# Kernel tuning notes

Measured on AMD Instinct MI355X. Metric: run time of the kernel, lower is better.

## Reference

```python
import jax, jax.numpy as jnp
import numpy as np

N, E = 100000, 3200000          # nodes, edges (avg degree 32)
F_IN, HID, OUT2, NUM_CLASSES = 128, 64, 2, 4


def setup_inputs() -> dict:
    key = jax.random.key(0)
    ks = jax.random.split(key, 8)
    x = jax.random.normal(ks[0], (N, F_IN), dtype=jnp.float32)
    edge_index = jax.random.randint(ks[1], (2, E), 0, N, dtype=jnp.int32)
    # Glorot-ish inits for the linear weights, zero biases (PyG GCNConv default)
    W1 = jax.random.normal(ks[2], (F_IN, HID), dtype=jnp.float32) / np.float32(np.sqrt(F_IN))
    b1 = jnp.zeros((HID,), jnp.float32)
    W2 = jax.random.normal(ks[3], (HID, OUT2), dtype=jnp.float32) / np.float32(np.sqrt(HID))
    b2 = jnp.zeros((OUT2,), jnp.float32)
    Wc = jax.random.normal(ks[4], (OUT2, NUM_CLASSES), dtype=jnp.float32) / np.float32(np.sqrt(OUT2))
    bc = jnp.zeros((NUM_CLASSES,), jnp.float32)
    return {"x": x, "edge_index": edge_index, "W1": W1, "b1": b1,
            "W2": W2, "b2": b2, "Wc": Wc, "bc": bc}


def gcn_conv(x, W, b, src, dst):
    """PyG GCNConv: out = D^-1/2 (A+I) D^-1/2 (x W) + b, sum aggregation."""
    n = x.shape[0]
    # degree of A+I: 1 (self loop) + in-degree at target nodes
    deg = jnp.ones((n,), x.dtype).at[dst].add(jnp.asarray(1.0, x.dtype))
    dinv = jax.lax.rsqrt(deg)                      # deg >= 1 always
    xw = x @ W                                      # [n, out] dense GEMM first
    norm = dinv[src] * dinv[dst]                    # [E]
    agg = jax.ops.segment_sum(xw[src] * norm[:, None], dst, num_segments=n)
    agg = agg + xw * (dinv * dinv)[:, None]         # self-loop contribution
    return agg + b


def reference(x, edge_index, W1, b1, W2, b2, Wc, bc):
    src, dst = edge_index[0], edge_index[1]
    h = jnp.tanh(gcn_conv(x, W1, b1, src, dst))
    h = jnp.tanh(gcn_conv(h, W2, b2, src, dst))
    out = h @ Wc + bc
    return (out, h)
```

## Files before the change

### kernel.cpp

```cpp
#include <hip/hip_runtime.h>
#include <hip/hip_bf16.h>
#include <hip/hip_fp16.h>


#define NB2 256
#define CAP2 9472
#define MAXB 400
#define BIN_CHUNK 4096

__global__ __launch_bounds__(256) void k_bin(const int* __restrict__ src,
                                             const int* __restrict__ dst,
                                             int E, int nbuckets,
                                             int* __restrict__ binCnt,
                                             int* __restrict__ bins) {
    __shared__ int stageP[BIN_CHUNK];
    __shared__ unsigned short stageB[BIN_CHUNK];
    __shared__ int lcnt[MAXB];
    __shared__ int lbase[MAXB + 1];
    __shared__ int gbase[MAXB];
    __shared__ int lpos[MAXB];
    int base = blockIdx.x * BIN_CHUNK;
    if (base >= E) return;
    int cnt_here = min(BIN_CHUNK, E - base);

    for (int b = threadIdx.x; b < nbuckets; b += 256) lcnt[b] = 0;
    __syncthreads();

    int p_[16], b_[16];
    #pragma unroll
    for (int k = 0; k < 4; k++) {
        int e0 = base + (k * 256 + threadIdx.x) * 4;
        int s4[4], d4[4];
        if (e0 + 3 < E) {
            *reinterpret_cast<int4*>(s4) = *reinterpret_cast<const int4*>(src + e0);
            *reinterpret_cast<int4*>(d4) = *reinterpret_cast<const int4*>(dst + e0);
            #pragma unroll
            for (int j = 0; j < 4; j++) {
                int b = d4[j] >> 8;
                b_[4 * k + j] = b;
                p_[4 * k + j] = s4[j] | ((d4[j] & 255) << 17);
                atomicAdd(&lcnt[b], 1);
            }
        } else {
            #pragma unroll
            for (int j = 0; j < 4; j++) {
                int e = e0 + j;
                if (e < E) {
                    int s = src[e], d = dst[e];
                    int b = d >> 8;
                    b_[4 * k + j] = b;
                    p_[4 * k + j] = s | ((d & 255) << 17);
                    atomicAdd(&lcnt[b], 1);
                } else {
                    b_[4 * k + j] = -1;
                }
            }
        }
    }
    __syncthreads();

    if (threadIdx.x < 64) {
        int lane = threadIdx.x;
        int per = (nbuckets + 63) >> 6;
        int start = lane * per;
        int v[8];
        int s = 0;
        for (int i = 0; i < per; ++i) {
            int b = start + i;
            v[i] = (b < nbuckets) ? lcnt[b] : 0;
            s += v[i];
        }
        int run = s;
        #pragma unroll
        for (int off = 1; off < 64; off <<= 1) {
            int t = __shfl_up(run, off);
            if (lane >= off) run += t;
        }
        int acc = run - s;
        for (int i = 0; i < per; ++i) {
            int b = start + i;
            if (b < nbuckets) lbase[b] = acc;
            acc += v[i];
        }
        if (lane == 63) lbase[nbuckets] = run;
    }
    __syncthreads();
    for (int b = threadIdx.x; b < nbuckets; b += 256) {
        gbase[b] = atomicAdd(&binCnt[b], lcnt[b]);
        lpos[b] = lbase[b];
    }
    __syncthreads();
    #pragma unroll
    for (int k = 0; k < 16; k++) {
        if (b_[k] >= 0) {
            int pos = atomicAdd(&lpos[b_[k]], 1);
            stageP[pos] = p_[k];
            stageB[pos] = (unsigned short)b_[k];
        }
    }
    __syncthreads();
    for (int i = threadIdx.x; i < cnt_here; i += 256) {
        int b = stageB[i];
        int gi = gbase[b] + (i - lbase[b]);
        if (gi < CAP2) bins[(size_t)b * CAP2 + gi] = stageP[i];
    }
}

__global__ void k_bscan(const int* __restrict__ binCnt, int* __restrict__ bbase,
                        int nbuckets, int* __restrict__ rowptr, int N) {
    int lane = threadIdx.x;
    int per = (nbuckets + 63) >> 6;
    int start = lane * per;
    int v[8];
    int s = 0;
    for (int i = 0; i < per; ++i) {
        int b = start + i;
        v[i] = (b < nbuckets) ? min(binCnt[b], CAP2) : 0;
        s += v[i];
    }
    int run = s;
    #pragma unroll
    for (int off = 1; off < 64; off <<= 1) {
        int t = __shfl_up(run, off);
        if (lane >= off) run += t;
    }
    int acc = run - s;
    for (int i = 0; i < per; ++i) {
        int b = start + i;
        if (b < nbuckets) bbase[b] = acc;
        acc += v[i];
    }
    if (lane == 63) {
        bbase[nbuckets] = run;
        rowptr[N] = run;
    }
}

__global__ __launch_bounds__(256) void k_csr(const int* __restrict__ bins,
                                             const int* __restrict__ binCnt,
                                             const int* __restrict__ bbase,
                                             int* __restrict__ rowptr,
                                             int* __restrict__ csr_src,
                                             float* __restrict__ dinv, int N) {
    __shared__ int hist[NB2];
    __shared__ int sc[NB2];
    __shared__ int lcur[NB2];
    __shared__ int stage[CAP2];
    int b = blockIdx.x;
    int lo = b * NB2;
    int nn = min(NB2, N - lo);
    if (nn <= 0) return;
    int m = min(binCnt[b], CAP2);
    const int* bp = bins + (size_t)b * CAP2;
    int t = threadIdx.x;

    hist[t] = 0;
    __syncthreads();
    for (int i = t; i < m; i += 256) {
        unsigned int e = (unsigned int)__builtin_nontemporal_load(bp + i);
        atomicAdd(&hist[e >> 17], 1);
    }
    __syncthreads();
    int h = (t < nn) ? hist[t] : 0;
    sc[t] = h;
    __syncthreads();
    #pragma unroll
    for (int off = 1; off < 256; off <<= 1) {
        int val = sc[t];
        int add = (t >= off) ? sc[t - off] : 0;
        __syncthreads();
        sc[t] = val + add;
        __syncthreads();
    }
    int excl = sc[t] - h;
    int gb = bbase[b];
    if (t < nn) {
        rowptr[lo + t] = gb + excl;
        lcur[t] = excl;
        dinv[lo + t] = rsqrtf(1.0f + (float)h);
    }
    __syncthreads();
    for (int i = t; i < m; i += 256) {
        unsigned int e = (unsigned int)__builtin_nontemporal_load(bp + i);
        int p = atomicAdd(&lcur[e >> 17], 1);
        stage[p] = (int)(e & 0x1FFFF);
    }
    __syncthreads();
    for (int i = t; i < m; i += 256) {
        csr_src[gb + i] = stage[i];
    }
}

__global__ __launch_bounds__(256) void k_gemm1(const float* __restrict__ x,
                                               const float* __restrict__ W1,
                                               const float* __restrict__ dinv,
                                               __half* __restrict__ xw, int n) {
    int lrow = threadIdx.x & 63;
    int c0 = __builtin_amdgcn_readfirstlane((threadIdx.x >> 6) * 16);
    int row = blockIdx.x * 64 + lrow;
    if (row > n) return;
    if (row == n) {
        float4 z = make_float4(0.f, 0.f, 0.f, 0.f);
        float4* op = reinterpret_cast<float4*>(xw + (size_t)row * 64 + c0);
        op[0] = z;
        op[1] = z;
        return;
    }
    const float* xr = x + (size_t)row * 128;

    float acc[16];
    #pragma unroll
    for (int c = 0; c < 16; ++c) acc[c] = 0.f;

    for (int k4 = 0; k4 < 32; ++k4) {
        float4 xv = *reinterpret_cast<const float4*>(xr + k4 * 4);
        const float* wp = W1 + (size_t)k4 * 4 * 64 + c0;
        #pragma unroll
        for (int c = 0; c < 16; ++c) {
            acc[c] = fmaf(xv.x, wp[c], acc[c]);
            acc[c] = fmaf(xv.y, wp[64 + c], acc[c]);
            acc[c] = fmaf(xv.z, wp[128 + c], acc[c]);
            acc[c] = fmaf(xv.w, wp[192 + c], acc[c]);
        }
    }

    float di = dinv[row];
    __half2 hb[8];
    #pragma unroll
    for (int c = 0; c < 8; ++c)
        hb[c] = __floats2half2_rn(acc[2 * c] * di, acc[2 * c + 1] * di);
    float4* op = reinterpret_cast<float4*>(xw + (size_t)row * 64 + c0);
    const float4* hp = reinterpret_cast<const float4*>(hb);
    op[0] = hp[0];
    op[1] = hp[1];
}

__global__ void k_agg1(const int* __restrict__ rowptr, const int* __restrict__ csr_src,
                       const float* __restrict__ dinv, const __half* __restrict__ xw1s,
                       const float* __restrict__ b1, const float* __restrict__ W2,
                       float* __restrict__ xw2s, int n) {
    int lane = threadIdx.x & 63;
    int q    = lane >> 4;
    int ln   = lane & 15;
    float4 b1v = *reinterpret_cast<const float4*>(b1 + 4 * ln);
    float4 w2a = *reinterpret_cast<const float4*>(W2 + 8 * ln);
    float4 w2b = *reinterpret_cast<const float4*>(W2 + 8 * ln + 4);
    const float2* xp2 = reinterpret_cast<const float2*>(xw1s);

    int wid  = blockIdx.x * (blockDim.x >> 6) + (threadIdx.x >> 6);
    int wtot = gridDim.x * (blockDim.x >> 6);
    int nquad = (n + 3) >> 2;
    for (int qd = wid; qd < nquad; qd += wtot) {
        int d = 4 * qd + q;
        bool ok = d < n;
        int base = 0, cnt = 0;
        float dd = 0.f;
        if (ok) { base = rowptr[d]; cnt = rowptr[d + 1] - base; dd = dinv[d]; }
        float a0 = 0.f, a1 = 0.f, a2 = 0.f, a3 = 0.f;

        int nch = (cnt + 15) >> 4;
        int ncm = max(nch, __shfl_xor(nch, 16));
        ncm = max(ncm, __shfl_xor(ncm, 32));

        for (int c = 0; c < ncm; ++c) {
            int rel = c * 16 + ln;
            int v = (rel < cnt) ? __builtin_nontemporal_load(csr_src + base + rel) : n;
            float2 r[16];
            #pragma unroll
            for (int k = 0; k < 16; ++k) {
                int sv = __shfl(v, (q << 4) | k);
                r[k] = xp2[(size_t)sv * 16 + ln];
            }
            __builtin_amdgcn_sched_barrier(0);
            #pragma unroll
            for (int k = 0; k < 16; ++k) {
                float2 f01 = __half22float2(__builtin_bit_cast(__half2, r[k].x));
                float2 f23 = __half22float2(__builtin_bit_cast(__half2, r[k].y));
                a0 += f01.x;
                a1 += f01.y;
                a2 += f23.x;
                a3 += f23.y;
            }
        }

        float p0 = 0.f, p1 = 0.f;
        if (ok) {
            float2 r = xp2[(size_t)d * 16 + ln];
            float2 s01 = __half22float2(__builtin_bit_cast(__half2, r.x));
            float2 s23 = __half22float2(__builtin_bit_cast(__half2, r.y));
            float h0 = tanhf((a0 + s01.x) * dd + b1v.x);
            float h1 = tanhf((a1 + s01.y) * dd + b1v.y);
            float h2 = tanhf((a2 + s23.x) * dd + b1v.z);
            float h3 = tanhf((a3 + s23.y) * dd + b1v.w);
            p0 = h0 * w2a.x + h1 * w2a.z + h2 * w2b.x + h3 * w2b.z;
            p1 = h0 * w2a.y + h1 * w2a.w + h2 * w2b.y + h3 * w2b.w;
        }
        #pragma unroll
        for (int m = 8; m >= 1; m >>= 1) {
            p0 += __shfl_xor(p0, m);
            p1 += __shfl_xor(p1, m);
        }
        if (ok && ln == 0)
            *reinterpret_cast<float2*>(xw2s + (size_t)d * 2) = make_float2(p0 * dd, p1 * dd);
    }
}

__global__ void k_agg2(const int* __restrict__ rowptr, const int* __restrict__ csr_src,
                       const float* __restrict__ dinv, const float* __restrict__ xw2s,
                       const float* __restrict__ b2, const float* __restrict__ Wc,
                       const float* __restrict__ bc,
                       float* __restrict__ out, float* __restrict__ hout, int n) {
    int lane = threadIdx.x & 63;
    int slot = lane >> 1;
    int f = lane & 1;
    float b2v = b2[f];
    int wid = blockIdx.x * (blockDim.x >> 6) + (threadIdx.x >> 6);
    int wtot = gridDim.x * (blockDim.x >> 6);
    for (int d = wid; d < n; d += wtot) {
        int base = rowptr[d], end = rowptr[d + 1];
        float dd = dinv[d];
        float acc = (slot == 0) ? xw2s[(size_t)d * 2 + f] : 0.f;
        for (int j = base + slot; j < end; j += 32) {
            int s = __builtin_nontemporal_load(csr_src + j);
            acc += xw2s[(size_t)s * 2 + f];
        }
        #pragma unroll
        for (int m = 32; m >= 2; m >>= 1) acc += __shfl_xor(acc, m);
        float h = tanhf(acc * dd + b2v);
        float other = __shfl_xor(h, 1);
        if (lane == 0) {
            *reinterpret_cast<float2*>(hout + (size_t)d * 2) = make_float2(h, other);
            float4 o;
            o.x = fmaf(h, Wc[0], fmaf(other, Wc[4], bc[0]));
            o.y = fmaf(h, Wc[1], fmaf(other, Wc[5], bc[1]));
            o.z = fmaf(h, Wc[2], fmaf(other, Wc[6], bc[2]));
            o.w = fmaf(h, Wc[3], fmaf(other, Wc[7], bc[3]));
            *reinterpret_cast<float4*>(out + (size_t)d * 4) = o;
        }
    }
}

extern "C" void kernel_launch(void* const* d_in, const int* in_sizes, int n_in,
                              void* d_out, int out_size, void* d_ws, size_t ws_size,
                              hipStream_t stream) {
    const float* x  = (const float*)d_in[0];
    const int* ei   = (const int*)d_in[1];
    const float* W1 = (const float*)d_in[2];
    const float* b1 = (const float*)d_in[3];
    const float* W2 = (const float*)d_in[4];
    const float* b2 = (const float*)d_in[5];
    const float* Wc = (const float*)d_in[6];
    const float* bc = (const float*)d_in[7];

    const int N = in_sizes[0] / 128;
    const int E = in_sizes[1] / 2;
    const int* src = ei;
    const int* dst = ei + E;

    float* out  = (float*)d_out;
    float* hout = out + (size_t)N * 4;

    const int NBK = (N + NB2 - 1) / NB2;

    char* ws = (char*)d_ws;
    int*    csr_src = (int*)ws;
    char*   uni     = (char*)(csr_src + E);
    int*    bins    = (int*)uni;
    __half* xw1s    = (__half*)uni;
    size_t uni_sz   = (size_t)NBK * CAP2 * sizeof(int);
    size_t xw1_sz   = (size_t)(N + 1) * 64 * sizeof(__half);
    char*  after    = uni + (uni_sz > xw1_sz ? uni_sz : xw1_sz);
    int*   binCnt   = (int*)after;
    int*   bbase    = binCnt + NBK;
    float* dinv     = (float*)(bbase + NBK + 1);
    float* xw2s     = dinv + N;
    int*   rowptr   = (int*)(xw2s + (size_t)N * 2);

    (void)hipMemsetAsync(binCnt, 0, (size_t)NBK * sizeof(int), stream);
    k_bin<<<(E + BIN_CHUNK - 1) / BIN_CHUNK, 256, 0, stream>>>(src, dst, E, NBK, binCnt, bins);
    k_bscan<<<1, 64, 0, stream>>>(binCnt, bbase, NBK, rowptr, N);
    k_csr<<<NBK, 256, 0, stream>>>(bins, binCnt, bbase, rowptr, csr_src, dinv, N);

    k_gemm1<<<(N + 64) / 64, 256, 0, stream>>>(x, W1, dinv, xw1s, N);
    k_agg1<<<2048, 256, 0, stream>>>(rowptr, csr_src, dinv, xw1s, b1, W2, xw2s, N);
    k_agg2<<<2048, 256, 0, stream>>>(rowptr, csr_src, dinv, xw2s, b2, Wc, bc, out, hout, N);
}
```

Before: 188.7 us.

## Sort nodes by degree within buckets for balanced aggregation; widen binning blocks

k_csr now builds a per-bucket counting sort of destination nodes by in-degree (dperm), and k_agg1 processes nodes in that order. Each wavefront's four node groups then have similar edge counts, which cuts idle lanes in the chunk loop where all quarters run to the maximum chunk count. Separately, k_bin moves to 512-thread blocks over 8192-edge chunks, giving fewer blocks and fewer global atomic merges per bucket. The costs are an extra scan in k_csr, an extra indirection load in k_agg1, scattered rather than sequential node access in k_agg1, and more shared memory in k_bin.

```diff
diff --git a/kernel.cpp b/kernel.cpp
--- a/kernel.cpp
+++ b/kernel.cpp
@@ -6,9 +6,9 @@
 #define NB2 256
 #define CAP2 9472
 #define MAXB 400
-#define BIN_CHUNK 4096
-
-__global__ __launch_bounds__(256) void k_bin(const int* __restrict__ src,
+#define BIN_CHUNK 8192
+
+__global__ __launch_bounds__(512) void k_bin(const int* __restrict__ src,
                                              const int* __restrict__ dst,
                                              int E, int nbuckets,
                                              int* __restrict__ binCnt,
@@ -23,13 +23,13 @@
     if (base >= E) return;
     int cnt_here = min(BIN_CHUNK, E - base);
 
-    for (int b = threadIdx.x; b < nbuckets; b += 256) lcnt[b] = 0;
+    for (int b = threadIdx.x; b < nbuckets; b += 512) lcnt[b] = 0;
     __syncthreads();
 
     int p_[16], b_[16];
     #pragma unroll
     for (int k = 0; k < 4; k++) {
-        int e0 = base + (k * 256 + threadIdx.x) * 4;
+        int e0 = base + (k * 512 + threadIdx.x) * 4;
         int s4[4], d4[4];
         if (e0 + 3 < E) {
             *reinterpret_cast<int4*>(s4) = *reinterpret_cast<const int4*>(src + e0);
@@ -85,7 +85,7 @@
         if (lane == 63) lbase[nbuckets] = run;
     }
     __syncthreads();
-    for (int b = threadIdx.x; b < nbuckets; b += 256) {
+    for (int b = threadIdx.x; b < nbuckets; b += 512) {
         gbase[b] = atomicAdd(&binCnt[b], lcnt[b]);
         lpos[b] = lbase[b];
     }
@@ -99,7 +99,7 @@
         }
     }
     __syncthreads();
-    for (int i = threadIdx.x; i < cnt_here; i += 256) {
+    for (int i = threadIdx.x; i < cnt_here; i += 512) {
         int b = stageB[i];
         int gi = gbase[b] + (i - lbase[b]);
         if (gi < CAP2) bins[(size_t)b * CAP2 + gi] = stageP[i];
@@ -141,10 +141,13 @@
                                              const int* __restrict__ bbase,
                                              int* __restrict__ rowptr,
                                              int* __restrict__ csr_src,
-                                             float* __restrict__ dinv, int N) {
+                                             float* __restrict__ dinv,
+                                             int* __restrict__ dperm, int N) {
     __shared__ int hist[NB2];
     __shared__ int sc[NB2];
     __shared__ int lcur[NB2];
+    __shared__ int dh[NB2];
+    __shared__ int dcur[NB2];
     __shared__ int stage[CAP2];
     int b = blockIdx.x;
     int lo = b * NB2;
@@ -155,6 +158,8 @@
     int t = threadIdx.x;
 
     hist[t] = 0;
+    dh[t] = 0;
+    dcur[t] = 0;
     __syncthreads();
     for (int i = t; i < m; i += 256) {
         unsigned int e = (unsigned int)__builtin_nontemporal_load(bp + i);
@@ -162,6 +167,8 @@
     }
     __syncthreads();
     int h = (t < nn) ? hist[t] : 0;
+    int g = min(h, 255);
+    if (t < nn) atomicAdd(&dh[g], 1);
     sc[t] = h;
     __syncthreads();
     #pragma unroll
@@ -180,6 +187,25 @@
         dinv[lo + t] = rsqrtf(1.0f + (float)h);
     }
     __syncthreads();
+
+    int dval = dh[t];
+    sc[t] = dval;
+    __syncthreads();
+    #pragma unroll
+    for (int off = 1; off < 256; off <<= 1) {
+        int val = sc[t];
+        int add = (t >= off) ? sc[t - off] : 0;
+        __syncthreads();
+        sc[t] = val + add;
+        __syncthreads();
+    }
+    dh[t] = sc[t] - dval;
+    __syncthreads();
+    if (t < nn) {
+        int pos = dh[g] + atomicAdd(&dcur[g], 1);
+        dperm[lo + pos] = lo + t;
+    }
+
     for (int i = t; i < m; i += 256) {
         unsigned int e = (unsigned int)__builtin_nontemporal_load(bp + i);
         int p = atomicAdd(&lcur[e >> 17], 1);
@@ -238,6 +264,7 @@
 __global__ void k_agg1(const int* __restrict__ rowptr, const int* __restrict__ csr_src,
                        const float* __restrict__ dinv, const __half* __restrict__ xw1s,
                        const float* __restrict__ b1, const float* __restrict__ W2,
+                       const int* __restrict__ dperm,
                        float* __restrict__ xw2s, int n) {
     int lane = threadIdx.x & 63;
     int q    = lane >> 4;
@@ -251,8 +278,9 @@
     int wtot = gridDim.x * (blockDim.x >> 6);
     int nquad = (n + 3) >> 2;
     for (int qd = wid; qd < nquad; qd += wtot) {
-        int d = 4 * qd + q;
-        bool ok = d < n;
+        int di0 = 4 * qd + q;
+        bool ok = di0 < n;
+        int d = ok ? dperm[di0] : 0;
         int base = 0, cnt = 0;
         float dd = 0.f;
         if (ok) { base = rowptr[d]; cnt = rowptr[d + 1] - base; dd = dinv[d]; }
@@ -375,13 +403,14 @@
     float* dinv     = (float*)(bbase + NBK + 1);
     float* xw2s     = dinv + N;
     int*   rowptr   = (int*)(xw2s + (size_t)N * 2);
+    int*   dperm    = rowptr + N + 1;
 
     (void)hipMemsetAsync(binCnt, 0, (size_t)NBK * sizeof(int), stream);
-    k_bin<<<(E + BIN_CHUNK - 1) / BIN_CHUNK, 256, 0, stream>>>(src, dst, E, NBK, binCnt, bins);
+    k_bin<<<(E + BIN_CHUNK - 1) / BIN_CHUNK, 512, 0, stream>>>(src, dst, E, NBK, binCnt, bins);
     k_bscan<<<1, 64, 0, stream>>>(binCnt, bbase, NBK, rowptr, N);
-    k_csr<<<NBK, 256, 0, stream>>>(bins, binCnt, bbase, rowptr, csr_src, dinv, N);
+    k_csr<<<NBK, 256, 0, stream>>>(bins, binCnt, bbase, rowptr, csr_src, dinv, dperm, N);
 
     k_gemm1<<<(N + 64) / 64, 256, 0, stream>>>(x, W1, dinv, xw1s, N);
-    k_agg1<<<2048, 256, 0, stream>>>(rowptr, csr_src, dinv, xw1s, b1, W2, xw2s, N);
+    k_agg1<<<2048, 256, 0, stream>>>(rowptr, csr_src, dinv, xw1s, b1, W2, dperm, xw2s, N);
     k_agg2<<<2048, 256, 0, stream>>>(rowptr, csr_src, dinv, xw2s, b2, Wc, bc, out, hout, N);
 }
```

Result: no change. 192.0 us (+1.8%).
